# Performance work log

Measured on AMD Instinct MI355X. Metric: run time of the kernel, lower is better.

Reference implementation:

```python
import jax, jax.numpy as jnp
import numpy as np

B, NQ, T = 1, 16, 512
L, D, H, HD, FF = 8, 512, 8, 64, 2048
LAT, CB, CBD = 1024, 2048, 256


def _rms(x, w, eps=1e-6):
    xf = x.astype(jnp.float32)
    y = xf * jax.lax.rsqrt(jnp.mean(xf * xf, axis=-1, keepdims=True) + eps)
    return y.astype(x.dtype) * w


def _rot_half(x):
    x1, x2 = jnp.split(x, 2, axis=-1)
    return jnp.concatenate((-x2, x1), axis=-1)


def _conv(x, w, b, pad):
    # x: [B, W, Cin], w: [K, Cin, Cout]
    return jax.lax.conv_general_dilated(x, w, (1,), pad, dimension_numbers=('NWC', 'WIO', 'NWC')) + b


def _convT(x, w, b, s):
    # output length = input length * s (SAME-padded transposed conv)
    return jax.lax.conv_transpose(x, w, (s,), 'SAME', dimension_numbers=('NWC', 'WIO', 'NWC')) + b


def setup_inputs() -> dict:
    key = jax.random.key(0)
    ks = iter(jax.random.split(key, 64))
    p = lambda *s: 0.02 * jax.random.normal(next(ks), s, jnp.float32)
    return dict(
        codes=jax.random.randint(next(ks), (B, NQ, T), 0, CB),
        emb_first=p(CB, CBD), pf_w=p(CBD, LAT), pf_b=p(LAT),
        fo_w=p(LAT, LAT), fo_b=p(LAT),
        emb_rest=p(NQ - 1, CB, CBD), pr_w=p(NQ - 1, CBD, LAT), pr_b=p(NQ - 1, LAT),
        ro_w=p(LAT, LAT), ro_b=p(LAT),
        pre_w=p(3, LAT, LAT), pre_b=p(LAT),
        in_w=p(LAT, D), in_b=p(D),
        ln1=jnp.ones((L, D)), qw=p(L, D, D), kw=p(L, D, D), vw=p(L, D, D), ow=p(L, D, D),
        qn=jnp.ones((L, HD)), kn=jnp.ones((L, HD)),
        ls_a=jnp.full((L, D), 0.1), ln2=jnp.ones((L, D)),
        w1=p(L, D, FF), w2=p(L, FF, D), ls_m=jnp.full((L, D), 0.1),
        fn_w=jnp.ones((D,)), out_w=p(D, LAT), out_b=p(LAT),
        up_w=p(4, LAT, LAT), up_b=p(LAT),
        dec0_w=p(7, LAT, 512), dec0_b=p(512),
        dw1=p(16, 512, 256), db1=p(256),
        dw2=p(12, 256, 128), db2=p(128),
        dw3=p(10, 128, 64), db3=p(64),
        dw4=p(8, 64, 32), db4=p(32),
        fin_w=p(7, 32, 1), fin_b=p(1),
    )


def reference(codes, emb_first, pf_w, pf_b, fo_w, fo_b, emb_rest, pr_w, pr_b, ro_w, ro_b,
              pre_w, pre_b, in_w, in_b, ln1, qw, kw, vw, ow, qn, kn, ls_a, ln2, w1, w2,
              ls_m, fn_w, out_w, out_b, up_w, up_b, dec0_w, dec0_b,
              dw1, db1, dw2, db2, dw3, db3, dw4, db4, fin_w, fin_b):
    Bc, _, Tc = codes.shape
    # --- RVQ decode (unrolled codebook lookups + 1x1 output projections) ---
    qf = jnp.take(emb_first, codes[:, 0], axis=0)            # [B,T,CBD]
    qf = qf @ pf_w + pf_b                                    # project_out -> [B,T,LAT]
    qf = qf @ fo_w + fo_b                                    # first_output_proj
    codes_rest = jnp.swapaxes(codes[:, 1:], 0, 1)            # [NQ-1,B,T]
    g = jax.vmap(lambda e, c: jnp.take(e, c, axis=0))(emb_rest, codes_rest)  # [NQ-1,B,T,CBD]
    qr = jnp.einsum('nbtc,ncd->btd', g, pr_w) + jnp.sum(pr_b, axis=0)
    qr = qr @ ro_w + ro_b                                    # rest_output_proj
    hidden = qf + qr                                         # [B,T,LAT]
    # --- causal pre_conv (k=3, left pad) ---
    hidden = _conv(hidden, pre_w, pre_b, [(2, 0)])
    # --- pre_transformer: RoPE + qk-norm + layerscale, manual causal attention ---
    h = hidden @ in_w + in_b                                 # [B,T,D]
    pos = jnp.arange(Tc, dtype=jnp.float32)
    inv_freq = 1.0 / (10000.0 ** (jnp.arange(0, HD, 2, dtype=jnp.float32) / HD))
    freqs = pos[:, None] * inv_freq[None, :]                 # [T,HD/2]
    emb = jnp.concatenate((freqs, freqs), axis=-1)           # [T,HD]
    cos, sin = jnp.cos(emb), jnp.sin(emb)
    mask = jnp.triu(jnp.full((Tc, Tc), -jnp.inf, dtype=jnp.float32), k=1)
    scale = HD ** -0.5
    for l in range(L):
        x = _rms(h, ln1[l])
        q = _rms((x @ qw[l]).reshape(Bc, Tc, H, HD), qn[l]).transpose(0, 2, 1, 3)
        k = _rms((x @ kw[l]).reshape(Bc, Tc, H, HD), kn[l]).transpose(0, 2, 1, 3)
        v = (x @ vw[l]).reshape(Bc, Tc, H, HD).transpose(0, 2, 1, 3)
        q = q * cos + _rot_half(q) * sin
        k = k * cos + _rot_half(k) * sin
        scores = jnp.einsum('bhqd,bhkd->bhqk', q, k) * scale + mask
        a = jax.nn.softmax(scores.astype(jnp.float32), axis=-1).astype(x.dtype)
        o = jnp.einsum('bhqk,bhkd->bhqd', a, v).transpose(0, 2, 1, 3).reshape(Bc, Tc, D)
        h = h + ls_a[l] * (o @ ow[l])
        x = _rms(h, ln2[l])
        h = h + ls_m[l] * (jax.nn.gelu(x @ w1[l], approximate=False) @ w2[l])
    h = _rms(h, fn_w) @ out_w + out_b                        # [B,T,LAT]
    # --- upsample x2 ---
    x = jax.nn.elu(_convT(h, up_w, up_b, 2))
    x = _conv(x, dec0_w, dec0_b, 'SAME')
    for w, b, r in ((dw1, db1, 8), (dw2, db2, 6), (dw3, db3, 5), (dw4, db4, 4)):
        x = _convT(jax.nn.elu(x), w, b, r)
    x = _conv(jax.nn.elu(x), fin_w, fin_b, 'SAME')           # [B,S,1]
    return jnp.clip(jnp.swapaxes(x, 1, 2), -1.0, 1.0)        # [B,1,S]
```

## Files before the change

kernel.cpp:

```cpp
#include <hip/hip_runtime.h>
#include <hip/hip_bf16.h>
#include <math.h>

#define T_LEN 512
#define LAT   1024
#define D_DIM 512
#define NH    8
#define HD    64
#define FF_D  2048
#define NL    8
#define NQ    16

typedef _Float16 f16x4 __attribute__((ext_vector_type(4)));
typedef _Float16 f16x8 __attribute__((ext_vector_type(8)));
typedef float    f32x4 __attribute__((ext_vector_type(4)));

#define WS_QFPRE    0
#define WS_G        131072
#define WS_QF       2097152
#define WS_TA       2621440
#define WS_HIDG     3145728
#define WS_HID      3147776
#define WS_CONV     3672064
#define WS_H        4196352
// ... 57 lines not shown
    int r = (idx >> 8) & 15;
    int t = idx >> 12;
    if (t >= T_LEN) return;
    if (r == 0) {
        int code = codes[t];
        qf_pre[t * 256 + c] = emb_first[code * 256 + c];
    } else {
        int n = r - 1;
        int code = codes[(n + 1) * T_LEN + t];
        G[t * 3840 + n * 256 + c] = emb_rest[(n * 2048 + code) * 256 + c];
    }
}

__global__ void k_bias_sum(const float* __restrict__ pr_b, float* __restrict__ out) {
    int d = blockIdx.x * 256 + threadIdx.x;
    if (d >= LAT) return;
    float s = 0.f;
    for (int n = 0; n < NQ - 1; n++) s += pr_b[n * LAT + d];
    out[d] = s;
}

__global__ void k_rope_tab(float* __restrict__ tab) {
    int idx = blockIdx.x * 256 + threadIdx.x;
    int t = idx >> 5, dm = idx & 31;
    double inv = pow(10000.0, -(double)dm / 32.0);
    double ang = (double)t * inv;
    tab[idx] = (float)cos(ang);
    tab[16384 + idx] = (float)sin(ang);
}

__global__ __launch_bounds__(256) void k_wt16(const float* __restrict__ w,
                                              _Float16* __restrict__ bth,
                                              _Float16* __restrict__ btl,
                                              int Cin, int Cout, int s, int pad_a) {
    int K3 = 3 * Cin;
    int col = blockIdx.x * 64 + (threadIdx.x & 63);
    int rk0 = blockIdx.y * 128 + (threadIdx.x >> 6) * 32;
    if (rk0 >= K3) return;
    int p = col / Cout, co = col - p * Cout;
    int kk0 = (pad_a - p) % s;
    if (kk0 < 0) kk0 += s;
    int cp = (p + kk0 - pad_a) / s;
    size_t ob = (size_t)col * K3 + rk0;
    for (int rb = 0; rb < 32; rb += 4) {
        f16x4 h, l;
#pragma unroll
        for (int j2 = 0; j2 < 4; ++j2) {
            int rowk = rk0 + rb + j2;
            int j = rowk / Cin, ci = rowk - j * Cin;
            int d = j - 1;
            float v = 0.f;
            if (d == cp) v = w[((size_t)kk0 * Cin + ci) * Cout + co];
            else if (d == cp + 1) v = w[((size_t)(kk0 + s) * Cin + ci) * Cout + co];
            _Float16 hh = (_Float16)v;
            h[j2] = hh;
            l[j2] = (_Float16)(v - (float)hh);
        }
        *(f16x4*)(bth + ob + rb) = h;
        *(f16x4*)(btl + ob + rb) = l;
    }
}

__global__ __launch_bounds__(256) void k_bt16(const float* __restrict__ w,
                                              _Float16* __restrict__ bth,
                                              _Float16* __restrict__ btl,
                                              int K, int N) {
    int col = blockIdx.x * 64 + (threadIdx.x & 63);
    int rk0 = blockIdx.y * 128 + (threadIdx.x >> 6) * 32;
    size_t ob = (size_t)col * K + rk0;
    for (int rb = 0; rb < 32; rb += 4) {
        f16x4 h, l;
#pragma unroll
        for (int j2 = 0; j2 < 4; ++j2) {
            float v = w[(size_t)(rk0 + rb + j2) * N + col];
            _Float16 hh = (_Float16)v;
            h[j2] = hh;
            l[j2] = (_Float16)(v - (float)hh);
        }
        *(f16x4*)(bth + ob + rb) = h;
        *(f16x4*)(btl + ob + rb) = l;
    }
}

__device__ __forceinline__ float apply_act(float v, int act) {
    if (act == 1) return 0.5f * v * (1.0f + erff(v * 0.70710678118654752440f));
    if (act == 2) return v > 0.f ? v : expm1f(v);
    return v;
}

__global__ __launch_bounds__(256) void k_gemm16(const float* __restrict__ A, int lda,
                                                const _Float16* __restrict__ BTh,
                                                const _Float16* __restrict__ BTl, int ldb,
                                                const float* __restrict__ bias, unsigned bmask,
                                                float* __restrict__ C,
                                                float* __restrict__ part, long mn,
                                                int N, int klen, int act) {
    __shared__ _Float16 Ash[128 * 64];
    __shared__ _Float16 Asl[128 * 64];
    __shared__ _Float16 Bsh[64 * 64];
    __shared__ _Float16 Bsl[64 * 64];
    int tid = threadIdx.x;
    int m0 = blockIdx.x * 128, n0 = blockIdx.y * 64;
    int kz = blockIdx.z * klen;
    const float* Ab = A + kz;
    int lane = tid & 63, wv = tid >> 6;
    int wr = wv >> 1, wc = wv & 1;
    int fr = lane & 15, g = lane >> 4;

    f32x4 acc[4][2];
#pragma unroll
    for (int m = 0; m < 4; ++m)
#pragma unroll
        for (int n = 0; n < 2; ++n)
#pragma unroll
            for (int r = 0; r < 4; ++r) acc[m][n][r] = 0.f;

    int nk = klen >> 6;
    for (int t = 0; t < nk; ++t) {
        int k0 = t << 6;
#pragma unroll
        for (int i2 = 0; i2 < 8; ++i2) {
            int c = tid + 256 * i2;
            int row = c >> 4, kc = c & 15;
            float4 v = *(const float4*)(Ab + (size_t)(m0 + row) * lda + k0 + (kc << 2));
            f16x4 h, l;
            float vv[4] = {v.x, v.y, v.z, v.w};
#pragma unroll
            for (int j = 0; j < 4; ++j) {
                _Float16 hh = (_Float16)vv[j];
                h[j] = hh;
                l[j] = (_Float16)(vv[j] - (float)hh);
            }
            int off = row * 64 + (((kc >> 1) ^ (row & 7)) << 3) + ((kc & 1) << 2);
            *(f16x4*)(Ash + off) = h;
            *(f16x4*)(Asl + off) = l;
        }
#pragma unroll
        for (int i2 = 0; i2 < 2; ++i2) {
            int c = tid + 256 * i2;
            int col = c >> 3, s = c & 7;
            size_t goff = (size_t)(n0 + col) * ldb + kz + k0 + (s << 3);
            f16x8 hv = *(const f16x8*)(BTh + goff);
            f16x8 lv = *(const f16x8*)(BTl + goff);
            int off = col * 64 + ((s ^ (col & 7)) << 3);
            *(f16x8*)(Bsh + off) = hv;
            *(f16x8*)(Bsl + off) = lv;
        }
        __syncthreads();
#pragma unroll
        for (int kk = 0; kk < 2; ++kk) {
            f16x8 ah[4], al[4], bh[2], bl[2];
#pragma unroll
            for (int m = 0; m < 4; ++m) {
                int row = wr * 64 + m * 16 + fr;
                int off = row * 64 + ((((kk << 2) + g) ^ (row & 7)) << 3);
                ah[m] = *(const f16x8*)(Ash + off);
                al[m] = *(const f16x8*)(Asl + off);
            }
#pragma unroll
            for (int n = 0; n < 2; ++n) {
                int col = wc * 32 + n * 16 + fr;
                int off = col * 64 + ((((kk << 2) + g) ^ (col & 7)) << 3);
                bh[n] = *(const f16x8*)(Bsh + off);
                bl[n] = *(const f16x8*)(Bsl + off);
            }
#pragma unroll
            for (int m = 0; m < 4; ++m)
#pragma unroll
                for (int n = 0; n < 2; ++n) {
                    acc[m][n] = __builtin_amdgcn_mfma_f32_16x16x32_f16(ah[m], bh[n], acc[m][n], 0, 0, 0);
                    acc[m][n] = __builtin_amdgcn_mfma_f32_16x16x32_f16(ah[m], bl[n], acc[m][n], 0, 0, 0);
                    acc[m][n] = __builtin_amdgcn_mfma_f32_16x16x32_f16(al[m], bh[n], acc[m][n], 0, 0, 0);
                }
        }
        __syncthreads();
    }
    if (part) {
        float* op = part + (size_t)blockIdx.z * mn;
#pragma unroll
        for (int m = 0; m < 4; ++m) {
            int row = m0 + wr * 64 + m * 16 + (g << 2);
#pragma unroll
            for (int n = 0; n < 2; ++n) {
                int col = n0 + wc * 32 + n * 16 + fr;
#pragma unroll
                for (int r = 0; r < 4; ++r)
                    op[(size_t)(row + r) * N + col] = acc[m][n][r];
            }
        }
    } else {
#pragma unroll
        for (int m = 0; m < 4; ++m) {
            int row = m0 + wr * 64 + m * 16 + (g << 2);
#pragma unroll
            for (int n = 0; n < 2; ++n) {
                int col = n0 + wc * 32 + n * 16 + fr;
                float bv = bias ? bias[col & bmask] : 0.f;
#pragma unroll
                for (int r = 0; r < 4; ++r) {
                    float v = acc[m][n][r] + bv;
                    v = apply_act(v, act);
                    C[(size_t)(row + r) * N + col] = v;
                }
            }
        }
    }
}

template <int NT>
__global__ __launch_bounds__(256) void k_gemm16h(
        const _Float16* __restrict__ Ah, const _Float16* __restrict__ Al, int lda,
        const _Float16* __restrict__ BTh, const _Float16* __restrict__ BTl, int ldb,
        const float* __restrict__ bias, unsigned bmask,
        float* __restrict__ C, _Float16* __restrict__ Ch, _Float16* __restrict__ Cl,
        float* __restrict__ part, long mn, int N, int klen, int act) {
    constexpr int BN = NT * 32;
    __shared__ _Float16 Ash[128 * 64];
    __shared__ _Float16 Asl[128 * 64];
    __shared__ _Float16 Bsh[BN * 64];
    __shared__ _Float16 Bsl[BN * 64];
    int tid = threadIdx.x;
    int m0 = blockIdx.x * 128, n0 = blockIdx.y * BN;
    int kz = blockIdx.z * klen;
    int lane = tid & 63, wv = tid >> 6;
    int wr = wv >> 1, wc = wv & 1;
    int fr = lane & 15, g = lane >> 4;

    f32x4 acc[4][NT];
#pragma unroll
    for (int m = 0; m < 4; ++m)
#pragma unroll
        for (int n = 0; n < NT; ++n)
#pragma unroll
            for (int r = 0; r < 4; ++r) acc[m][n][r] = 0.f;

    int nk = klen >> 6;
    for (int t = 0; t < nk; ++t) {
        int k0 = kz + (t << 6);
#pragma unroll
        for (int i2 = 0; i2 < 4; ++i2) {
            int c = tid + 256 * i2;
            int row = c >> 3, s = c & 7;
            size_t go = (size_t)(m0 + row) * lda + k0 + (s << 3);
            f16x8 hv = *(const f16x8*)(Ah + go);
            f16x8 lv = *(const f16x8*)(Al + go);
            int off = row * 64 + ((s ^ (row & 7)) << 3);
            *(f16x8*)(Ash + off) = hv;
            *(f16x8*)(Asl + off) = lv;
        }
#pragma unroll
        for (int i2 = 0; i2 < BN / 32; ++i2) {
            int c = tid + 256 * i2;
            int col = c >> 3, s = c & 7;
            size_t go = (size_t)(n0 + col) * ldb + k0 + (s << 3);
            f16x8 hv = *(const f16x8*)(BTh + go);
            f16x8 lv = *(const f16x8*)(BTl + go);
            int off = col * 64 + ((s ^ (col & 7)) << 3);
            *(f16x8*)(Bsh + off) = hv;
            *(f16x8*)(Bsl + off) = lv;
        }
        __syncthreads();
#pragma unroll
        for (int kk = 0; kk < 2; ++kk) {
            f16x8 ah[4], al4[4], bh[NT], bl[NT];
#pragma unroll
            for (int m = 0; m < 4; ++m) {
                int row = wr * 64 + m * 16 + fr;
                int off = row * 64 + ((((kk << 2) + g) ^ (row & 7)) << 3);
                ah[m] = *(const f16x8*)(Ash + off);
                al4[m] = *(const f16x8*)(Asl + off);
            }
#pragma unroll
            for (int n = 0; n < NT; ++n) {
                int col = wc * (NT * 16) + n * 16 + fr;
                int off = col * 64 + ((((kk << 2) + g) ^ (col & 7)) << 3);
                bh[n] = *(const f16x8*)(Bsh + off);
                bl[n] = *(const f16x8*)(Bsl + off);
            }
#pragma unroll
            for (int m = 0; m < 4; ++m)
#pragma unroll
                for (int n = 0; n < NT; ++n) {
                    acc[m][n] = __builtin_amdgcn_mfma_f32_16x16x32_f16(ah[m], bh[n], acc[m][n], 0, 0, 0);
                    acc[m][n] = __builtin_amdgcn_mfma_f32_16x16x32_f16(ah[m], bl[n], acc[m][n], 0, 0, 0);
                    acc[m][n] = __builtin_amdgcn_mfma_f32_16x16x32_f16(al4[m], bh[n], acc[m][n], 0, 0, 0);
                }
        }
// ... 57 lines not shown
#pragma unroll
    for (int i = 0; i < AR; i++) areg[i] = A[(size_t)(m0 + arow[i]) * lda + akk[i]];
#pragma unroll
    for (int i = 0; i < 4; i++) breg[i] = B[(size_t)(br0 + 4 * i) * N + n0 + bc];
#pragma unroll
    for (int i = 0; i < AR; i++) As[0][akk[i]][arow[i]] = areg[i];
#pragma unroll
    for (int i = 0; i < 4; i++) Bs[0][br0 + 4 * i][bc] = breg[i];
    __syncthreads();
    int nk = klen >> 4;
    for (int t = 0; t < nk; t++) {
        int cur = t & 1;
        if (t + 1 < nk) {
            int k0 = (t + 1) << 4;
#pragma unroll
            for (int i = 0; i < AR; i++) areg[i] = A[(size_t)(m0 + arow[i]) * lda + k0 + akk[i]];
#pragma unroll
            for (int i = 0; i < 4; i++) breg[i] = B[(size_t)(k0 + br0 + 4 * i) * N + n0 + bc];
        }
#pragma unroll
        for (int kk = 0; kk < 16; kk++) {
            float a[RM], b[4];
#pragma unroll
            for (int i = 0; i < RM; i++) a[i] = As[cur][kk][ty * RM + i];
#pragma unroll
            for (int j = 0; j < 4; j++) b[j] = Bs[cur][kk][tx * 4 + j];
#pragma unroll
            for (int i = 0; i < RM; i++)
#pragma unroll
                for (int j = 0; j < 4; j++) acc[i][j] += a[i] * b[j];
        }
        if (t + 1 < nk) {
            int nxt = cur ^ 1;
#pragma unroll
            for (int i = 0; i < AR; i++) As[nxt][akk[i]][arow[i]] = areg[i];
#pragma unroll
            for (int i = 0; i < 4; i++) Bs[nxt][br0 + 4 * i][bc] = breg[i];
            __syncthreads();
        }
    }
}

template <int TM>
__global__ __launch_bounds__(256) void k_gemm2(const float* __restrict__ A, int lda,
                                               const float* __restrict__ B,
                                               const float* __restrict__ bias, unsigned bmask,
                                               const float* __restrict__ res,
                                               const float* __restrict__ scale,
                                               float* __restrict__ C,
                                               float* __restrict__ part, long mn,
                                               int N, int klen, int act) {
    constexpr int RM = TM / 16;
    float acc[RM][4] = {};
    int m0 = blockIdx.x * TM, n0 = blockIdx.y * 64;
    int kz = blockIdx.z * klen;
    gemm_core<TM>(A + kz, lda, B + (size_t)kz * N, N, klen, m0, n0, acc);
    int tid = threadIdx.x;
    int tx = tid & 15, ty = tid >> 4;
    if (part) {
        float* out = part + (size_t)blockIdx.z * mn;
#pragma unroll
        for (int i = 0; i < RM; i++)
#pragma unroll
            for (int j = 0; j < 4; j++)
                out[(size_t)(m0 + ty * RM + i) * N + n0 + tx * 4 + j] = acc[i][j];
    } else {
#pragma unroll
        for (int i = 0; i < RM; i++) {
            int row = m0 + ty * RM + i;
#pragma unroll
            for (int j = 0; j < 4; j++) {
                int col = n0 + tx * 4 + j;
                float v = acc[i][j];
                if (bias) v += bias[col & bmask];
                v = apply_act(v, act);
                if (scale) v *= scale[col];
                if (res) v += res[(size_t)row * N + col];
                C[(size_t)row * N + col] = v;
            }
        }
    }
}

__global__ __launch_bounds__(256) void k_qkv(const float* __restrict__ A,
                                             const float* __restrict__ B0,
                                             const float* __restrict__ B1,
                                             const float* __restrict__ B2,
                                             float* __restrict__ part) {
    int which = blockIdx.z >> 1, s = blockIdx.z & 1;
    const float* B = which == 0 ? B0 : (which == 1 ? B1 : B2);
    float acc[2][4] = {};
    int m0 = blockIdx.x * 32, n0 = blockIdx.y * 64;
    int kz = s * 256;
    gemm_core<32>(A + kz, 512, B + (size_t)kz * 512, 512, 256, m0, n0, acc);
    int tid = threadIdx.x;
    int tx = tid & 15, ty = tid >> 4;
    float* out = part + (size_t)blockIdx.z * (512 * 512);
#pragma unroll
    for (int i = 0; i < 2; i++)
#pragma unroll
        for (int j = 0; j < 4; j++)
            out[(size_t)(m0 + ty * 2 + i) * 512 + n0 + tx * 4 + j] = acc[i][j];
}

__global__ __launch_bounds__(256) void k_reduce(const float* __restrict__ part, long mn, int S,
                                                const float* __restrict__ bias, unsigned bmask,
                                                const float* __restrict__ res,
                                                const float* __restrict__ scale,
                                                float* __restrict__ C, int N, int act) {
    long idx = ((long)blockIdx.x * 256 + threadIdx.x) * 4;
    if (idx >= mn) return;
    float4 v = *(const float4*)(part + idx);
    for (int s2 = 1; s2 < S; s2++) {
        float4 u = *(const float4*)(part + (size_t)s2 * mn + idx);
        v.x += u.x; v.y += u.y; v.z += u.z; v.w += u.w;
    }
    int col = (int)(idx % N);
    float vv[4] = {v.x, v.y, v.z, v.w};
#pragma unroll
    for (int j = 0; j < 4; j++) {
        float t = vv[j];
        int c = col + j;
        if (bias) t += bias[c & bmask];
        t = apply_act(t, act);
        if (scale) t *= scale[c];
        if (res) t += res[idx + j];
        vv[j] = t;
    }
    *(float4*)(C + idx) = make_float4(vv[0], vv[1], vv[2], vv[3]);
}

__global__ __launch_bounds__(256) void k_reduce_h(const float* __restrict__ part, long mn, int S,
                                                  const float* __restrict__ bias, unsigned bmask,
                                                  _Float16* __restrict__ Ch,
                                                  _Float16* __restrict__ Cl, int N, int act) {
    long idx = ((long)blockIdx.x * 256 + threadIdx.x) * 4;
    if (idx >= mn) return;
    float4 v = *(const float4*)(part + idx);
    for (int s2 = 1; s2 < S; s2++) {
        float4 u = *(const float4*)(part + (size_t)s2 * mn + idx);
        v.x += u.x; v.y += u.y; v.z += u.z; v.w += u.w;
    }
    int col = (int)(idx % N);
    float vv[4] = {v.x, v.y, v.z, v.w};
    f16x4 h, l;
#pragma unroll
    for (int j = 0; j < 4; j++) {
        float t = vv[j];
        if (bias) t += bias[(col + j) & bmask];
        t = apply_act(t, act);
        _Float16 hh = (_Float16)t;
        h[j] = hh;
        l[j] = (_Float16)(t - (float)hh);
    }
    *(f16x4*)(Ch + idx) = h;
    *(f16x4*)(Cl + idx) = l;
}

__global__ __launch_bounds__(256) void k_reduce_qkv(const float* __restrict__ part,
                                                    float* __restrict__ q,
                                                    float* __restrict__ k,
                                                    float* __restrict__ v) {
    const long mn = 262144;
    int w = blockIdx.y;
    long idx = ((long)blockIdx.x * 256 + threadIdx.x) * 4;
    float4 a = *(const float4*)(part + (size_t)(2 * w) * mn + idx);
    float4 b = *(const float4*)(part + (size_t)(2 * w + 1) * mn + idx);
    float* C = w == 0 ? q : (w == 1 ? k : v);
    *(float4*)(C + idx) = make_float4(a.x + b.x, a.y + b.y, a.z + b.z, a.w + b.w);
}

__global__ __launch_bounds__(256) void k_rms(const float* __restrict__ x,
                                             const float* __restrict__ g,
                                             float* __restrict__ y, int N) {
    int row = blockIdx.x;
    const float* xr = x + (size_t)row * N;
    int tid = threadIdx.x;
    float s = 0.f;
    for (int i = tid; i < N; i += 256) { float v = xr[i]; s += v * v; }
#pragma unroll
    for (int off = 32; off; off >>= 1) s += __shfl_xor(s, off);
    __shared__ float red[4];
    if ((tid & 63) == 0) red[tid >> 6] = s;
    __syncthreads();
    s = red[0] + red[1] + red[2] + red[3];
    float r = 1.0f / sqrtf(s / (float)N + 1e-6f);
    for (int i = tid; i < N; i += 256) y[(size_t)row * N + i] = xr[i] * r * g[i];
// ... 135 lines not shown
        for (int dt = 0; dt < 4; ++dt) {
            const float* vp = v + (size_t)(c0 + g * 8) * 512 + hoff + dt * 16 + fr;
            f16x8 bh, bl;
#pragma unroll
            for (int j = 0; j < 8; ++j) {
                float x = vp[(size_t)j * 512];
                _Float16 hh = (_Float16)x;
                bh[j] = hh;
                bl[j] = (_Float16)(x - (float)hh);
            }
            accO[dt] = __builtin_amdgcn_mfma_f32_16x16x32_f16(pah, bh, accO[dt], 0, 0, 0);
            accO[dt] = __builtin_amdgcn_mfma_f32_16x16x32_f16(pah, bl, accO[dt], 0, 0, 0);
            accO[dt] = __builtin_amdgcn_mfma_f32_16x16x32_f16(pal, bh, accO[dt], 0, 0, 0);
        }
    }
    if (s == 1) {
        if (g == 0) { mM[fr] = m_run; lM[fr] = l_run; }
#pragma unroll
        for (int dt = 0; dt < 4; ++dt)
#pragma unroll
            for (int r = 0; r < 4; ++r)
                OM[g * 4 + r][dt * 16 + fr] = accO[dt][r];
    }
    __syncthreads();
    if (s == 0) {
        float m1 = mM[fr], l1 = lM[fr];
        float mf = fmaxf(m_run, m1);
        float a0 = __expf(m_run - mf), a1 = __expf(m1 - mf);
        float lf = l_run * a0 + l1 * a1;
        float inv = 1.0f / lf;
        float a0r[4], a1r[4], invr[4];
#pragma unroll
        for (int r = 0; r < 4; ++r) {
            a0r[r] = __shfl(a0, g * 4 + r);
            a1r[r] = __shfl(a1, g * 4 + r);
            invr[r] = __shfl(inv, g * 4 + r);
        }
#pragma unroll
        for (int dt = 0; dt < 4; ++dt)
#pragma unroll
            for (int r = 0; r < 4; ++r) {
                float ov = (accO[dt][r] * a0r[r] + OM[g * 4 + r][dt * 16 + fr] * a1r[r]) * invr[r];
                o[(size_t)(qr0 + g * 4 + r) * 512 + hoff + dt * 16 + fr] = ov;
            }
    }
}

__global__ __launch_bounds__(256) void k_conv_fin(const float* __restrict__ x,
                                                  const float* __restrict__ w,
                                                  const float* __restrict__ b,
                                                  float* __restrict__ y, int n) {
    __shared__ float xs[262 * 33];
    __shared__ float wsm[224];
    int tid = threadIdx.x;
    int o0 = blockIdx.x * 256;
    for (int i = tid; i < 262 * 32; i += 256) {
        int r = i >> 5, c = i & 31;
        int t = o0 - 3 + r;
        xs[r * 33 + c] = (t >= 0 && t < n) ? x[(size_t)t * 32 + c] : 0.f;
    }
    if (tid < 224) wsm[tid] = w[tid];
    __syncthreads();
    float acc = b[0];
#pragma unroll
    for (int kk = 0; kk < 7; kk++)
#pragma unroll
        for (int ci = 0; ci < 32; ci++)
            acc += xs[(tid + kk) * 33 + ci] * wsm[kk * 32 + ci];
    y[o0 + tid] = fminf(fmaxf(acc, -1.f), 1.f);
}

static inline void gemmS64(hipStream_t st, const float* A, int lda, const float* B,
                           const float* bias, unsigned bmask, const float* res,
                           const float* scale, float* C, float* part,
                           int M, int N, int K, int S, int act) {
    long mn = (long)M * N;
    if (S > 1) {
        k_gemm2<64><<<dim3(M / 64, N / 64, S), 256, 0, st>>>(
            A, lda, B, nullptr, 0, nullptr, nullptr, nullptr, part, mn, N, K / S, 0);
        k_reduce<<<dim3((int)(mn / 1024)), 256, 0, st>>>(
            part, mn, S, bias, bmask, res, scale, C, N, act);
    } else {
        k_gemm2<64><<<dim3(M / 64, N / 64, 1), 256, 0, st>>>(
            A, lda, B, bias, bmask, res, scale, C, nullptr, mn, N, K, act);
    }
}
static inline void gemmS32(hipStream_t st, const float* A, int lda, const float* B,
                           const float* bias, unsigned bmask, const float* res,
                           const float* scale, float* C, float* part,
                           int M, int N, int K, int S, int act) {
    long mn = (long)M * N;
    if (S > 1) {
        k_gemm2<32><<<dim3(M / 32, N / 64, S), 256, 0, st>>>(
            A, lda, B, nullptr, 0, nullptr, nullptr, nullptr, part, mn, N, K / S, 0);
        k_reduce<<<dim3((int)(mn / 1024)), 256, 0, st>>>(
            part, mn, S, bias, bmask, res, scale, C, N, act);
    } else {
        k_gemm2<32><<<dim3(M / 32, N / 64, 1), 256, 0, st>>>(
            A, lda, B, bias, bmask, res, scale, C, nullptr, mn, N, K, act);
    }
}

extern "C" void kernel_launch(void* const* d_in, const int* in_sizes, int n_in,
                              void* d_out, int out_size, void* d_ws, size_t ws_size,
                              hipStream_t stream) {
    int i = 0;
    const int*   codes     = (const int*)  d_in[i++];
    const float* emb_first = (const float*)d_in[i++];
    const float* pf_w      = (const float*)d_in[i++];
    const float* pf_b      = (const float*)d_in[i++];
    const float* fo_w      = (const float*)d_in[i++];
    const float* fo_b      = (const float*)d_in[i++];
    const float* emb_rest  = (const float*)d_in[i++];
    const float* pr_w      = (const float*)d_in[i++];
    const float* pr_b      = (const float*)d_in[i++];
    const float* ro_w      = (const float*)d_in[i++];
    const float* ro_b      = (const float*)d_in[i++];
    const float* pre_w     = (const float*)d_in[i++];
    const float* pre_b     = (const float*)d_in[i++];
    const float* in_w      = (const float*)d_in[i++];
    const float* in_b      = (const float*)d_in[i++];
    const float* ln1       = (const float*)d_in[i++];
    const float* qw        = (const float*)d_in[i++];
    const float* kw        = (const float*)d_in[i++];
    const float* vw        = (const float*)d_in[i++];
    const float* ow        = (const float*)d_in[i++];
    const float* qn        = (const float*)d_in[i++];
    const float* kn        = (const float*)d_in[i++];
    const float* ls_a      = (const float*)d_in[i++];
    const float* ln2       = (const float*)d_in[i++];
    const float* w1        = (const float*)d_in[i++];
    const float* w2        = (const float*)d_in[i++];
    const float* ls_m      = (const float*)d_in[i++];
    const float* fn_w      = (const float*)d_in[i++];
    const float* out_w     = (const float*)d_in[i++];
    const float* out_b     = (const float*)d_in[i++];
    const float* up_w      = (const float*)d_in[i++];
    const float* up_b      = (const float*)d_in[i++];
    const float* dec0_w    = (const float*)d_in[i++];
    const float* dec0_b    = (const float*)d_in[i++];
    const float* dw1       = (const float*)d_in[i++];
    const float* db1       = (const float*)d_in[i++];
    const float* dw2       = (const float*)d_in[i++];
    const float* db2       = (const float*)d_in[i++];
    const float* dw3       = (const float*)d_in[i++];
    const float* db3       = (const float*)d_in[i++];
    const float* dw4       = (const float*)d_in[i++];
    const float* db4       = (const float*)d_in[i++];
    const float* fin_w     = (const float*)d_in[i++];
    const float* fin_b     = (const float*)d_in[i++];

    float* ws = (float*)d_ws;
    float* outp = (float*)d_out;

    float* qf_pre   = ws + WS_QFPRE;
    float* G        = ws + WS_G;
    float* qf       = ws + WS_QF;
    float* tA       = ws + WS_TA;
    float* hidden   = ws + WS_HID;
    float* conv_out = ws + WS_CONV;
    float* h        = ws + WS_H;
    float* x        = ws + WS_X;
    float* qb       = ws + WS_QB;
    float* kb       = ws + WS_KB;
    float* vb       = ws + WS_VB;
    float* attnb    = ws + WS_ATT;
    float* ff       = ws + WS_FF;
    float* bias_sum = ws + WS_BSUM;
    float* houtp    = ws + WS_HOUT;
    float* t4       = ws + WS_T4;
    float* part     = ws + WS_PART;
    float* ropetab  = ws + WS_ROPE;

    _Float16* up16h = (_Float16*)(ws + UP16H_D);
    _Float16* up16l = (_Float16*)(ws + UP16L_D);
    _Float16* dec16h = (_Float16*)(ws + DEC16H_D);
    _Float16* dec16l = (_Float16*)(ws + DEC16L_D);
    _Float16* t1h = (_Float16*)(ws + T1H_D);
    _Float16* t1l = (_Float16*)(ws + T1L_D);
    _Float16* t2h = (_Float16*)(ws + T2H_D);
    _Float16* t2l = (_Float16*)(ws + T2L_D);
    _Float16* t3h = (_Float16*)(ws + T3H_D);
    _Float16* t3l = (_Float16*)(ws + T3L_D);

    _Float16* BTup_h = (_Float16*)(ws + WS_W2UP);   _Float16* BTup_l = BTup_h + 2048 * 3072;
    _Float16* BTd1_h = (_Float16*)(ws + WS_W2D1);   _Float16* BTd1_l = BTd1_h + 2048 * 1536;
    _Float16* BTd2_h = (_Float16*)(ws + WS_W2D2);   _Float16* BTd2_l = BTd2_h + 768 * 768;
    _Float16* BTd3_h = (_Float16*)(ws + WS_W2D3);   _Float16* BTd3_l = BTd3_h + 320 * 384;
    _Float16* BTd4_h = (_Float16*)(ws + WS_W2D4);   _Float16* BTd4_l = BTd4_h + 128 * 192;
    _Float16* BTd0_h = (_Float16*)(ws + WS_DEC0B16);_Float16* BTd0_l = BTd0_h + 512 * 7168;
    _Float16* BTpr_h = (_Float16*)(ws + WS_BTPR);   _Float16* BTpr_l = BTpr_h + 1024 * 3840;

    k_zero_guards<<<15, 256, 0, stream>>>(ws);
    k_rope_tab<<<64, 256, 0, stream>>>(ropetab);
    k_wt16<<<dim3(32, 24), 256, 0, stream>>>(up_w, BTup_h, BTup_l, 1024, 1024, 2, 2);
    k_wt16<<<dim3(32, 12), 256, 0, stream>>>(dw1, BTd1_h, BTd1_l, 512, 256, 8, 11);
    k_wt16<<<dim3(12, 6), 256, 0, stream>>>(dw2, BTd2_h, BTd2_l, 256, 128, 6, 8);
    k_wt16<<<dim3(5, 3), 256, 0, stream>>>(dw3, BTd3_h, BTd3_l, 128, 64, 5, 7);
    k_wt16<<<dim3(2, 2), 256, 0, stream>>>(dw4, BTd4_h, BTd4_l, 64, 32, 4, 5);
    k_bt16<<<dim3(8, 56), 256, 0, stream>>>(dec0_w, BTd0_h, BTd0_l, 7168, 512);
    k_bt16<<<dim3(16, 30), 256, 0, stream>>>(pr_w, BTpr_h, BTpr_l, 3840, 1024);

    k_gather<<<8192, 256, 0, stream>>>(codes, emb_first, emb_rest, qf_pre, G);
    k_bias_sum<<<4, 256, 0, stream>>>(pr_b, bias_sum);
    gemmS64(stream, qf_pre, 256, pf_w, pf_b, ~0u, nullptr, nullptr, tA, part, 512, 1024, 256, 2, 0);
    gemmS64(stream, tA, 1024, fo_w, fo_b, ~0u, nullptr, nullptr, qf, part, 512, 1024, 1024, 4, 0);
    k_gemm16<<<dim3(4, 16, 4), 256, 0, stream>>>(G, 3840, BTpr_h, BTpr_l, 3840,
            nullptr, 0, nullptr, part, 524288L, 1024, 960, 0);
    k_reduce<<<512, 256, 0, stream>>>(part, 524288L, 4, bias_sum, ~0u, nullptr, nullptr,
            tA, 1024, 0);
    gemmS64(stream, tA, 1024, ro_w, ro_b, ~0u, qf, nullptr, hidden, part, 512, 1024, 1024, 4, 0);

    gemmS64(stream, hidden - 2048, 1024, pre_w, pre_b, ~0u, nullptr, nullptr,
            conv_out, part, 512, 1024, 3072, 8, 0);

    gemmS32(stream, conv_out, 1024, in_w, in_b, ~0u, nullptr, nullptr, h, part, 512, 512, 1024, 4, 0);

    for (int l = 0; l < NL; l++) {
        const float* qw_l = qw + (size_t)l * D_DIM * D_DIM;
        const float* kw_l = kw + (size_t)l * D_DIM * D_DIM;
        const float* vw_l = vw + (size_t)l * D_DIM * D_DIM;
        const float* ow_l = ow + (size_t)l * D_DIM * D_DIM;
        const float* w1_l = w1 + (size_t)l * D_DIM * FF_D;
        const float* w2_l = w2 + (size_t)l * FF_D * D_DIM;

        k_rms<<<512, 256, 0, stream>>>(h, ln1 + l * D_DIM, x, D_DIM);
        k_qkv<<<dim3(16, 8, 6), 256, 0, stream>>>(x, qw_l, kw_l, vw_l, part);
        k_reduce_qkv<<<dim3(256, 3), 256, 0, stream>>>(part, qb, kb, vb);
        k_qkrope2<<<dim3(T_LEN * NH, 2), 64, 0, stream>>>(qb, kb, qn + l * HD, kn + l * HD, ropetab);
        k_attn_mf<<<256, 128, 0, stream>>>(qb, kb, vb, attnb);
        gemmS32(stream, attnb, 512, ow_l, nullptr, 0, h, ls_a + l * D_DIM, h, part,
                512, 512, 512, 2, 0);
        k_rms<<<512, 256, 0, stream>>>(h, ln2 + l * D_DIM, x, D_DIM);
        gemmS64(stream, x, 512, w1_l, nullptr, 0, nullptr, nullptr, ff, part,
                512, 2048, 512, 2, 1);
        gemmS32(stream, ff, 2048, w2_l, nullptr, 0, h, ls_m + l * D_DIM, h, part,
                512, 512, 2048, 8, 0);
    }

    k_rms<<<512, 256, 0, stream>>>(h, fn_w, x, D_DIM);
    gemmS64(stream, x, 512, out_w, out_b, ~0u, nullptr, nullptr, houtp, part, 512, 1024, 512, 4, 0);

    k_gemm16<<<dim3(4, 32, 2), 256, 0, stream>>>(houtp - 1024, 1024, BTup_h, BTup_l, 3072,
            nullptr, 0, nullptr, part, 1048576L, 2048, 1536, 0);
    k_reduce_h<<<1024, 256, 0, stream>>>(part, 1048576L, 2, up_b, 1023u,
            up16h, up16l, 2048, 2);

    k_gemm16h<4><<<dim3(8, 4, 8), 256, 0, stream>>>(up16h - 3072, up16l - 3072, 1024,
            BTd0_h, BTd0_l, 7168, nullptr, 0, nullptr, nullptr, nullptr,
            part, 524288L, 512, 896, 0);
    k_reduce_h<<<512, 256, 0, stream>>>(part, 524288L, 8, dec0_b, ~0u,
            dec16h, dec16l, 512, 2);
    k_zero2<<<8, 256, 0, stream>>>(ws);

    k_gemm16h<2><<<dim3(8, 32, 1), 256, 0, stream>>>(dec16h - 512, dec16l - 512, 512,
            BTd1_h, BTd1_l, 1536, db1, 255u, nullptr, t1h, t1l, nullptr, 0L, 2048, 1536, 2);
    k_gemm16h<4><<<dim3(64, 6, 1), 256, 0, stream>>>(t1h - 256, t1l - 256, 256,
            BTd2_h, BTd2_l, 768, db2, 127u, nullptr, t2h, t2l, nullptr, 0L, 768, 768, 2);
    k_gemm16h<2><<<dim3(384, 5, 1), 256, 0, stream>>>(t2h - 128, t2l - 128, 128,
            BTd3_h, BTd3_l, 384, db3, 63u, nullptr, t3h, t3l, nullptr, 0L, 320, 384, 2);
    k_gemm16h<4><<<dim3(1920, 1, 1), 256, 0, stream>>>(t3h - 64, t3l - 64, 64,
            BTd4_h, BTd4_l, 192, db4, 31u, t4, nullptr, nullptr, nullptr, 0L, 128, 192, 2);

    k_conv_fin<<<983040 / 256, 256, 0, stream>>>(t4, fin_w, fin_b, outp, 983040);
}
```

Before: 2.006 ms.

## Move transformer and projection GEMMs to split-fp16 MFMA with per-layer weight conversion

Result: faster. 1.898 ms (-5.4%).

```diff
diff --git a/kernel.cpp b/kernel.cpp
--- a/kernel.cpp
+++ b/kernel.cpp
@@ -163,10 +163,124 @@
     }
 }
 
+__global__ __launch_bounds__(256) void k_ltw(const float* __restrict__ qw,
+                                             const float* __restrict__ kw,
+                                             const float* __restrict__ vw,
+                                             const float* __restrict__ ow,
+                                             const float* __restrict__ w1,
+                                             const float* __restrict__ w2,
+                                             _Float16* __restrict__ LW) {
+    int b = blockIdx.x;
+    const float* src; _Float16 *dh, *dl; int K, N, colb, rkb;
+    if (b < 128) {
+        int which = b >> 5, sub = b & 31;
+        src = which == 0 ? qw : which == 1 ? kw : which == 2 ? vw : ow;
+        K = 512; N = 512; colb = sub & 7; rkb = sub >> 3;
+        dh = LW + which * 524288; dl = dh + 262144;
+    } else if (b < 256) {
+        int sub = b - 128;
+        src = w1; K = 512; N = 2048; colb = sub & 31; rkb = sub >> 5;
+        dh = LW + 2097152; dl = LW + 3145728;
+    } else {
+        int sub = b - 256;
+        src = w2; K = 2048; N = 512; colb = sub & 7; rkb = sub >> 3;
+        dh = LW + 4194304; dl = LW + 5242880;
+    }
+    int tid = threadIdx.x;
+    int col = colb * 64 + (tid & 63);
+    int rk0 = rkb * 128 + (tid >> 6) * 32;
+    size_t ob = (size_t)col * K + rk0;
+    for (int rb = 0; rb < 32; rb += 8) {
+        f16x8 h, l;
+#pragma unroll
+        for (int j = 0; j < 8; ++j) {
+            float v = src[(size_t)(rk0 + rb + j) * N + col];
+            _Float16 hh = (_Float16)v;
+            h[j] = hh;
+            l[j] = (_Float16)(v - (float)hh);
+        }
+        *(f16x8*)(dh + ob + rb) = h;
+        *(f16x8*)(dl + ob + rb) = l;
+    }
+}
+
 __device__ __forceinline__ float apply_act(float v, int act) {
     if (act == 1) return 0.5f * v * (1.0f + erff(v * 0.70710678118654752440f));
     if (act == 2) return v > 0.f ? v : expm1f(v);
     return v;
+}
+
+__device__ __forceinline__ void mf_core(const float* __restrict__ Ab, int lda,
+                                        const _Float16* __restrict__ BTh,
+                                        const _Float16* __restrict__ BTl, int ldb,
+                                        int m0, int n0, int kz, int klen,
+                                        f32x4 (&acc)[4][2],
+                                        _Float16* Ash, _Float16* Asl,
+                                        _Float16* Bsh, _Float16* Bsl) {
+    int tid = threadIdx.x;
+    int lane = tid & 63, wv = tid >> 6;
+    int wr = wv >> 1, wc = wv & 1;
+    int fr = lane & 15, g = lane >> 4;
+    int nk = klen >> 6;
+    for (int t = 0; t < nk; ++t) {
+        int k0 = t << 6;
+#pragma unroll
+        for (int i2 = 0; i2 < 8; ++i2) {
+            int c = tid + 256 * i2;
+            int row = c >> 4, kc = c & 15;
+            float4 v = *(const float4*)(Ab + (size_t)(m0 + row) * lda + k0 + (kc << 2));
+            f16x4 h, l;
+            float vv[4] = {v.x, v.y, v.z, v.w};
+#pragma unroll
+            for (int j = 0; j < 4; ++j) {
+                _Float16 hh = (_Float16)vv[j];
+                h[j] = hh;
+                l[j] = (_Float16)(vv[j] - (float)hh);
+            }
+            int off = row * 64 + (((kc >> 1) ^ (row & 7)) << 3) + ((kc & 1) << 2);
+            *(f16x4*)(Ash + off) = h;
+            *(f16x4*)(Asl + off) = l;
+        }
+#pragma unroll
+        for (int i2 = 0; i2 < 2; ++i2) {
+            int c = tid + 256 * i2;
+            int col = c >> 3, s = c & 7;
+            size_t goff = (size_t)(n0 + col) * ldb + kz + k0 + (s << 3);
+            f16x8 hv = *(const f16x8*)(BTh + goff);
+            f16x8 lv = *(const f16x8*)(BTl + goff);
+            int off = col * 64 + ((s ^ (col & 7)) << 3);
+            *(f16x8*)(Bsh + off) = hv;
+            *(f16x8*)(Bsl + off) = lv;
+        }
+        __syncthreads();
+#pragma unroll
+        for (int kk = 0; kk < 2; ++kk) {
+            f16x8 ah[4], al[4], bh[2], bl[2];
+#pragma unroll
+            for (int m = 0; m < 4; ++m) {
+                int row = wr * 64 + m * 16 + fr;
+                int off = row * 64 + ((((kk << 2) + g) ^ (row & 7)) << 3);
+                ah[m] = *(const f16x8*)(Ash + off);
+                al[m] = *(const f16x8*)(Asl + off);
+            }
+#pragma unroll
+            for (int n = 0; n < 2; ++n) {
+                int col = wc * 32 + n * 16 + fr;
+                int off = col * 64 + ((((kk << 2) + g) ^ (col & 7)) << 3);
+                bh[n] = *(const f16x8*)(Bsh + off);
+                bl[n] = *(const f16x8*)(Bsl + off);
+            }
+#pragma unroll
+            for (int m = 0; m < 4; ++m)
+#pragma unroll
+                for (int n = 0; n < 2; ++n) {
+                    acc[m][n] = __builtin_amdgcn_mfma_f32_16x16x32_f16(ah[m], bh[n], acc[m][n], 0, 0, 0);
+                    acc[m][n] = __builtin_amdgcn_mfma_f32_16x16x32_f16(ah[m], bl[n], acc[m][n], 0, 0, 0);
+                    acc[m][n] = __builtin_amdgcn_mfma_f32_16x16x32_f16(al[m], bh[n], acc[m][n], 0, 0, 0);
+                }
+        }
+        __syncthreads();
+    }
 }
 
 __global__ __launch_bounds__(256) void k_gemm16(const float* __restrict__ A, int lda,
@@ -180,82 +294,20 @@
     __shared__ _Float16 Asl[128 * 64];
     __shared__ _Float16 Bsh[64 * 64];
     __shared__ _Float16 Bsl[64 * 64];
-    int tid = threadIdx.x;
     int m0 = blockIdx.x * 128, n0 = blockIdx.y * 64;
     int kz = blockIdx.z * klen;
-    const float* Ab = A + kz;
+    f32x4 acc[4][2];
+#pragma unroll
+    for (int m = 0; m < 4; ++m)
+#pragma unroll
+        for (int n = 0; n < 2; ++n)
+#pragma unroll
+            for (int r = 0; r < 4; ++r) acc[m][n][r] = 0.f;
+    mf_core(A + kz, lda, BTh, BTl, ldb, m0, n0, kz, klen, acc, Ash, Asl, Bsh, Bsl);
+    int tid = threadIdx.x;
     int lane = tid & 63, wv = tid >> 6;
     int wr = wv >> 1, wc = wv & 1;
     int fr = lane & 15, g = lane >> 4;
-
-    f32x4 acc[4][2];
-#pragma unroll
-    for (int m = 0; m < 4; ++m)
-#pragma unroll
-        for (int n = 0; n < 2; ++n)
-#pragma unroll
-            for (int r = 0; r < 4; ++r) acc[m][n][r] = 0.f;
-
-    int nk = klen >> 6;
-    for (int t = 0; t < nk; ++t) {
-        int k0 = t << 6;
-#pragma unroll
-        for (int i2 = 0; i2 < 8; ++i2) {
-            int c = tid + 256 * i2;
-            int row = c >> 4, kc = c & 15;
-            float4 v = *(const float4*)(Ab + (size_t)(m0 + row) * lda + k0 + (kc << 2));
-            f16x4 h, l;
-            float vv[4] = {v.x, v.y, v.z, v.w};
-#pragma unroll
-            for (int j = 0; j < 4; ++j) {
-                _Float16 hh = (_Float16)vv[j];
-                h[j] = hh;
-                l[j] = (_Float16)(vv[j] - (float)hh);
-            }
-            int off = row * 64 + (((kc >> 1) ^ (row & 7)) << 3) + ((kc & 1) << 2);
-            *(f16x4*)(Ash + off) = h;
-            *(f16x4*)(Asl + off) = l;
-        }
-#pragma unroll
-        for (int i2 = 0; i2 < 2; ++i2) {
-            int c = tid + 256 * i2;
-            int col = c >> 3, s = c & 7;
-            size_t goff = (size_t)(n0 + col) * ldb + kz + k0 + (s << 3);
-            f16x8 hv = *(const f16x8*)(BTh + goff);
-            f16x8 lv = *(const f16x8*)(BTl + goff);
-            int off = col * 64 + ((s ^ (col & 7)) << 3);
-            *(f16x8*)(Bsh + off) = hv;
-            *(f16x8*)(Bsl + off) = lv;
-        }
-        __syncthreads();
-#pragma unroll
-        for (int kk = 0; kk < 2; ++kk) {
-            f16x8 ah[4], al[4], bh[2], bl[2];
-#pragma unroll
-            for (int m = 0; m < 4; ++m) {
-                int row = wr * 64 + m * 16 + fr;
-                int off = row * 64 + ((((kk << 2) + g) ^ (row & 7)) << 3);
-                ah[m] = *(const f16x8*)(Ash + off);
-                al[m] = *(const f16x8*)(Asl + off);
-            }
-#pragma unroll
-            for (int n = 0; n < 2; ++n) {
-                int col = wc * 32 + n * 16 + fr;
-                int off = col * 64 + ((((kk << 2) + g) ^ (col & 7)) << 3);
-                bh[n] = *(const f16x8*)(Bsh + off);
-                bl[n] = *(const f16x8*)(Bsl + off);
-            }
-#pragma unroll
-            for (int m = 0; m < 4; ++m)
-#pragma unroll
-                for (int n = 0; n < 2; ++n) {
-                    acc[m][n] = __builtin_amdgcn_mfma_f32_16x16x32_f16(ah[m], bh[n], acc[m][n], 0, 0, 0);
-                    acc[m][n] = __builtin_amdgcn_mfma_f32_16x16x32_f16(ah[m], bl[n], acc[m][n], 0, 0, 0);
-                    acc[m][n] = __builtin_amdgcn_mfma_f32_16x16x32_f16(al[m], bh[n], acc[m][n], 0, 0, 0);
-                }
-        }
-        __syncthreads();
-    }
     if (part) {
         float* op = part + (size_t)blockIdx.z * mn;
 #pragma unroll
@@ -284,6 +336,44 @@
                     C[(size_t)(row + r) * N + col] = v;
                 }
             }
+        }
+    }
+}
+
+__global__ __launch_bounds__(256) void k_qkv16(const float* __restrict__ A,
+                                               const _Float16* __restrict__ LW,
+                                               float* __restrict__ part) {
+    __shared__ _Float16 Ash[128 * 64];
+    __shared__ _Float16 Asl[128 * 64];
+    __shared__ _Float16 Bsh[64 * 64];
+    __shared__ _Float16 Bsl[64 * 64];
+    int which = blockIdx.z >> 1, s2 = blockIdx.z & 1;
+    const _Float16* BTh = LW + which * 524288;
+    const _Float16* BTl = BTh + 262144;
+    int m0 = blockIdx.x * 128, n0 = blockIdx.y * 64;
+    int kz = s2 * 256;
+    f32x4 acc[4][2];
+#pragma unroll
+    for (int m = 0; m < 4; ++m)
+#pragma unroll
+        for (int n = 0; n < 2; ++n)
+#pragma unroll
+            for (int r = 0; r < 4; ++r) acc[m][n][r] = 0.f;
+    mf_core(A + kz, 512, BTh, BTl, 512, m0, n0, kz, 256, acc, Ash, Asl, Bsh, Bsl);
+    int tid = threadIdx.x;
+    int lane = tid & 63, wv = tid >> 6;
+    int wr = wv >> 1, wc = wv & 1;
+    int fr = lane & 15, g = lane >> 4;
+    float* op = part + (size_t)blockIdx.z * 262144;
+#pragma unroll
+    for (int m = 0; m < 4; ++m) {
+        int row = m0 + wr * 64 + m * 16 + (g << 2);
+#pragma unroll
+        for (int n = 0; n < 2; ++n) {
+            int col = n0 + wc * 32 + n * 16 + fr;
+#pragma unroll
+            for (int r = 0; r < 4; ++r)
+                op[(size_t)(row + r) * 512 + col] = acc[m][n][r];
         }
     }
 }
@@ -507,27 +597,6 @@
     }
 }
 
-__global__ __launch_bounds__(256) void k_qkv(const float* __restrict__ A,
-                                             const float* __restrict__ B0,
-                                             const float* __restrict__ B1,
-                                             const float* __restrict__ B2,
-                                             float* __restrict__ part) {
-    int which = blockIdx.z >> 1, s = blockIdx.z & 1;
-    const float* B = which == 0 ? B0 : (which == 1 ? B1 : B2);
-    float acc[2][4] = {};
-    int m0 = blockIdx.x * 32, n0 = blockIdx.y * 64;
-    int kz = s * 256;
-    gemm_core<32>(A + kz, 512, B + (size_t)kz * 512, 512, 256, m0, n0, acc);
-    int tid = threadIdx.x;
-    int tx = tid & 15, ty = tid >> 4;
-    float* out = part + (size_t)blockIdx.z * (512 * 512);
-#pragma unroll
-    for (int i = 0; i < 2; i++)
-#pragma unroll
-        for (int j = 0; j < 4; j++)
-            out[(size_t)(m0 + ty * 2 + i) * 512 + n0 + tx * 4 + j] = acc[i][j];
-}
-
 __global__ __launch_bounds__(256) void k_reduce(const float* __restrict__ part, long mn, int S,
                                                 const float* __restrict__ bias, unsigned bmask,
                                                 const float* __restrict__ res,
@@ -829,21 +898,6 @@
             part, mn, S, bias, bmask, res, scale, C, N, act);
     } else {
         k_gemm2<64><<<dim3(M / 64, N / 64, 1), 256, 0, st>>>(
-            A, lda, B, bias, bmask, res, scale, C, nullptr, mn, N, K, act);
-    }
-}
-static inline void gemmS32(hipStream_t st, const float* A, int lda, const float* B,
-                           const float* bias, unsigned bmask, const float* res,
-                           const float* scale, float* C, float* part,
-                           int M, int N, int K, int S, int act) {
-    long mn = (long)M * N;
-    if (S > 1) {
-        k_gemm2<32><<<dim3(M / 32, N / 64, S), 256, 0, st>>>(
-            A, lda, B, nullptr, 0, nullptr, nullptr, nullptr, part, mn, N, K / S, 0);
-        k_reduce<<<dim3((int)(mn / 1024)), 256, 0, st>>>(
-            part, mn, S, bias, bmask, res, scale, C, N, act);
-    } else {
-        k_gemm2<32><<<dim3(M / 32, N / 64, 1), 256, 0, st>>>(
             A, lda, B, bias, bmask, res, scale, C, nullptr, mn, N, K, act);
     }
 }
@@ -938,6 +992,8 @@
     _Float16* BTd0_h = (_Float16*)(ws + WS_DEC0B16);_Float16* BTd0_l = BTd0_h + 512 * 7168;
     _Float16* BTpr_h = (_Float16*)(ws + WS_BTPR);   _Float16* BTpr_l = BTpr_h + 1024 * 3840;
 
+    _Float16* LW = (_Float16*)ws;
+
     k_zero_guards<<<15, 256, 0, stream>>>(ws);
     k_rope_tab<<<64, 256, 0, stream>>>(ropetab);
     k_wt16<<<dim3(32, 24), 256, 0, stream>>>(up_w, BTup_h, BTup_l, 1024, 1024, 2, 2);
@@ -958,10 +1014,17 @@
             tA, 1024, 0);
     gemmS64(stream, tA, 1024, ro_w, ro_b, ~0u, qf, nullptr, hidden, part, 512, 1024, 1024, 4, 0);
 
-    gemmS64(stream, hidden - 2048, 1024, pre_w, pre_b, ~0u, nullptr, nullptr,
-            conv_out, part, 512, 1024, 3072, 8, 0);
-
-    gemmS32(stream, conv_out, 1024, in_w, in_b, ~0u, nullptr, nullptr, h, part, 512, 512, 1024, 4, 0);
+    k_bt16<<<dim3(16, 24), 256, 0, stream>>>(pre_w, LW, LW + 3145728, 3072, 1024);
+    k_gemm16<<<dim3(4, 16, 4), 256, 0, stream>>>(hidden - 2048, 1024, LW, LW + 3145728, 3072,
+            nullptr, 0, nullptr, part, 524288L, 1024, 768, 0);
+    k_reduce<<<512, 256, 0, stream>>>(part, 524288L, 4, pre_b, ~0u, nullptr, nullptr,
+            conv_out, 1024, 0);
+
+    k_bt16<<<dim3(8, 8), 256, 0, stream>>>(in_w, LW, LW + 524288, 1024, 512);
+    k_gemm16<<<dim3(4, 8, 2), 256, 0, stream>>>(conv_out, 1024, LW, LW + 524288, 1024,
+            nullptr, 0, nullptr, part, 262144L, 512, 512, 0);
+    k_reduce<<<256, 256, 0, stream>>>(part, 262144L, 2, in_b, ~0u, nullptr, nullptr,
+            h, 512, 0);
 
     for (int l = 0; l < NL; l++) {
         const float* qw_l = qw + (size_t)l * D_DIM * D_DIM;
@@ -971,22 +1034,29 @@
         const float* w1_l = w1 + (size_t)l * D_DIM * FF_D;
         const float* w2_l = w2 + (size_t)l * FF_D * D_DIM;
 
+        k_ltw<<<384, 256, 0, stream>>>(qw_l, kw_l, vw_l, ow_l, w1_l, w2_l, LW);
         k_rms<<<512, 256, 0, stream>>>(h, ln1 + l * D_DIM, x, D_DIM);
-        k_qkv<<<dim3(16, 8, 6), 256, 0, stream>>>(x, qw_l, kw_l, vw_l, part);
+        k_qkv16<<<dim3(4, 8, 6), 256, 0, stream>>>(x, LW, part);
         k_reduce_qkv<<<dim3(256, 3), 256, 0, stream>>>(part, qb, kb, vb);
         k_qkrope2<<<dim3(T_LEN * NH, 2), 64, 0, stream>>>(qb, kb, qn + l * HD, kn + l * HD, ropetab);
         k_attn_mf<<<256, 128, 0, stream>>>(qb, kb, vb, attnb);
-        gemmS32(stream, attnb, 512, ow_l, nullptr, 0, h, ls_a + l * D_DIM, h, part,
-                512, 512, 512, 2, 0);
+        k_gemm16<<<dim3(4, 8, 2), 256, 0, stream>>>(attnb, 512, LW + 1572864, LW + 1835008, 512,
+                nullptr, 0, nullptr, part, 262144L, 512, 256, 0);
+        k_reduce<<<256, 256, 0, stream>>>(part, 262144L, 2, nullptr, 0, h, ls_a + l * D_DIM,
+                h, 512, 0);
         k_rms<<<512, 256, 0, stream>>>(h, ln2 + l * D_DIM, x, D_DIM);
-        gemmS64(stream, x, 512, w1_l, nullptr, 0, nullptr, nullptr, ff, part,
-                512, 2048, 512, 2, 1);
-        gemmS32(stream, ff, 2048, w2_l, nullptr, 0, h, ls_m + l * D_DIM, h, part,
-                512, 512, 2048, 8, 0);
+        k_gemm16<<<dim3(4, 32, 1), 256, 0, stream>>>(x, 512, LW + 2097152, LW + 3145728, 512,
+                nullptr, 0, ff, nullptr, 0L, 2048, 512, 1);
+        k_gemm16<<<dim3(4, 8, 4), 256, 0, stream>>>(ff, 2048, LW + 4194304, LW + 5242880, 2048,
+                nullptr, 0, nullptr, part, 262144L, 512, 512, 0);
+        k_reduce<<<256, 256, 0, stream>>>(part, 262144L, 4, nullptr, 0, h, ls_m + l * D_DIM,
+                h, 512, 0);
     }
 
     k_rms<<<512, 256, 0, stream>>>(h, fn_w, x, D_DIM);
-    gemmS64(stream, x, 512, out_w, out_b, ~0u, nullptr, nullptr, houtp, part, 512, 1024, 512, 4, 0);
+    k_bt16<<<dim3(16, 4), 256, 0, stream>>>(out_w, LW, LW + 524288, 512, 1024);
+    k_gemm16<<<dim3(4, 16, 1), 256, 0, stream>>>(x, 512, LW, LW + 524288, 512,
+            out_b, ~0u, houtp, nullptr, 0L, 1024, 512, 0);
 
     k_gemm16<<<dim3(4, 32, 2), 256, 0, stream>>>(houtp - 1024, 1024, BTup_h, BTup_l, 3072,
             nullptr, 0, nullptr, part, 1048576L, 2048, 1536, 0);
```
